# Optimization experiments

Measured on AMD Instinct MI355X. Metric: run time of the kernel, lower is better.

## Reference

```python
import jax, jax.numpy as jnp
import numpy as np

B, W, N = 4, 8, 1024
F_IN, HID, OUT = 256, 256, 128


def setup_inputs() -> dict:
    key = jax.random.key(0)
    ks = jax.random.split(key, 8)
    X = jax.random.normal(ks[0], (B, W, N, F_IN), dtype=jnp.float32)
    adj = jax.random.uniform(ks[1], (B, W, N, N), dtype=jnp.float32)
    # Linear params, torch default init: U(-1/sqrt(fan_in), 1/sqrt(fan_in))
    def lin(k, fi, fo):
        k1, k2 = jax.random.split(k)
        bnd = 1.0 / np.sqrt(fi)
        Wm = jax.random.uniform(k1, (fi, fo), minval=-bnd, maxval=bnd, dtype=jnp.float32)
        bm = jax.random.uniform(k2, (fo,), minval=-bnd, maxval=bnd, dtype=jnp.float32)
        return Wm, bm
    W1, b1 = lin(ks[2], F_IN, HID)
    W2, b2 = lin(ks[3], HID, HID)
    W3, b3 = lin(ks[4], HID, OUT)
    return {"X": X, "adj": adj, "W1": W1, "b1": b1, "W2": W2, "b2": b2, "W3": W3, "b3": b3}


def _normalize(adj):
    # adj: [B, W, N, N]. adj_hat = adj + I; sym degree norm D^-1/2 A D^-1/2
    n = adj.shape[-1]
    adj_hat = adj + jnp.eye(n, dtype=adj.dtype)
    d = jnp.sum(adj_hat, axis=-1) ** (-0.5)            # [B, W, N]
    # diag(d) @ adj_hat @ diag(d) == row/col scaling (same math, no N^3 diag matmuls)
    return adj_hat * d[..., :, None] * d[..., None, :]


def reference(X, adj, W1, b1, W2, b2, W3, b3):
    adj_norm = _normalize(adj)                          # [B, W, N, N]
    h = X
    for Wm, bm in ((W1, b1), (W2, b2), (W3, b3)):
        h = jnp.einsum('bwnm,bwmf->bwnf', adj_norm, h)  # aggregate
        h = jax.nn.relu(jnp.einsum('bwnf,fo->bwno', h, Wm) + bm)
    return h                                            # [B, W, N, OUT]
```

## Files before the change

### kernel.cpp

```cpp
#include <hip/hip_runtime.h>
#include <hip/hip_bf16.h>
#include <cstdint>
#include <cstddef>

#define NN 1024
#define FF 256

typedef __attribute__((ext_vector_type(8))) short bf16x8;
typedef __attribute__((ext_vector_type(4))) float f32x4;

__device__ __forceinline__ short f2bf(float x) {
  unsigned int u = __float_as_uint(x);
  u = (u + 0x7fffu + ((u >> 16) & 1u)) >> 16;
  return (short)u;
}


__global__ __launch_bounds__(256)
void dinv_cast(const float* __restrict__ adj, float* __restrict__ dinv,
               short* __restrict__ Ahat) {
  __shared__ float wsum[64];
  int b = blockIdx.x;
  int bw = b >> 6, s = b & 63;
  int t = threadIdx.x;
  int wid = t >> 6, lane = t & 63;
  int row = lane & 15;
  int rloc = (s << 4) + row;
  int kg = (lane >> 4) & 3;
  const float* arow = adj + ((size_t)(bw << 10) + rloc) * NN;
  short* outb = Ahat + ((size_t)bw << 20) + ((size_t)s << 14) + (t << 3);
  float ssum = 0.f;
  #pragma unroll
  for (int it = 0; it < 8; it++) {
    int col = (it << 7) + (wid << 5) + (kg << 3);
    float4 a0 = *(const float4*)(arow + col);
    float4 a1 = *(const float4*)(arow + col + 4);
    float v[8] = {a0.x, a0.y, a0.z, a0.w, a1.x, a1.y, a1.z, a1.w};
    union { ushort o[8]; int4 q; } pk;
    #pragma unroll
    for (int j = 0; j < 8; j++) {
      v[j] += (rloc == col + j) ? 1.f : 0.f;
      ssum += v[j];
      pk.o[j] = (ushort)f2bf(v[j]);
    }
    *(int4*)(outb + (it << 11)) = pk.q;
  }
  ssum += __shfl_down(ssum, 32, 64);
  ssum += __shfl_down(ssum, 16, 64);
  if (lane < 16) wsum[(wid << 4) + lane] = ssum;
  __syncthreads();
  if (t < 16) {
    float tot = wsum[t] + wsum[16 + t] + wsum[32 + t] + wsum[48 + t];
    dinv[(bw << 10) + (s << 4) + t] = rsqrtf(tot);
  }
}

__global__ __launch_bounds__(256)
void transpose_x(const float* __restrict__ X, const float* __restrict__ dinv,
                 short* __restrict__ XT) {
  __shared__ short T[64][72];
  int bwo = blockIdx.z;
  int n0 = blockIdx.x << 6, f0 = blockIdx.y << 6;
  int t = threadIdx.x;
  {
    int n = t >> 2, fc = (t & 3) << 4;
    float dn = dinv[(bwo << 10) + n0 + n];
    const float* src = X + (((size_t)bwo * NN + n0 + n) * FF) + f0 + fc;
    #pragma unroll
    for (int i = 0; i < 4; i++) {
      float4 v = ((const float4*)src)[i];
      ushort4 p;
      p.x = (unsigned short)f2bf(v.x * dn); p.y = (unsigned short)f2bf(v.y * dn);
      p.z = (unsigned short)f2bf(v.z * dn); p.w = (unsigned short)f2bf(v.w * dn);
      *(ushort4*)&T[n][fc + (i << 2)] = p;
    }
  }
  __syncthreads();
  {
    int f = t >> 2, nc = (t & 3) << 4;
    int fg = f0 + f, ng = n0 + nc;
    short tmp[16];
    #pragma unroll
    for (int i = 0; i < 16; i++) tmp[i] = T[nc + i][f];
    size_t e0 = ((size_t)bwo << 18) + ((size_t)(fg >> 4) << 14) + ((ng >> 5) << 9)
              + (((ng & 31) >> 3) << 7) + ((fg & 15) << 3);
    *(int4*)(XT + e0)       = *(int4*)&tmp[0];
    *(int4*)(XT + e0 + 128) = *(int4*)&tmp[8];
  }
}

__global__ __launch_bounds__(256)
void transpose_w(const float* __restrict__ W, short* __restrict__ WT, int FO) {
  int idx = blockIdx.x * 256 + threadIdx.x;
  if (idx >= FO * 256) return;
  int fo = idx >> 8, fi = idx & 255;
  size_t e = (size_t)((fo >> 4) << 12) + ((fi >> 5) << 9)
           + (((fi & 31) >> 3) << 7) + ((fo & 15) << 3) + (fi & 7);
  WT[e] = f2bf(W[fi * FO + fo]);
}

template<int F_OUT, bool FINAL>
__global__ __launch_bounds__(256, 3)
void gcn_layer(const short* __restrict__ Ahat,
               const float* __restrict__ dinv,
               const short* __restrict__ Gin,
               const short* __restrict__ WT,
               const float* __restrict__ bias,
               short* __restrict__ Gout,
               float* __restrict__ Out) {
  __shared__ short aggL[64 * 272];

  int b = blockIdx.x;
  int x = b & 7, m = b >> 3;
  int bw = (x << 2) + (m >> 4);
  int rb = m & 15;
  int r0 = rb << 6;

  int tid = threadIdx.x;
  int wf = tid >> 6, lane = tid & 63;
  int l15 = lane & 15, l4 = lane >> 4;

  const short* Hbase = Gin  + ((size_t)bw << 18) + ((size_t)(wf << 2) << 14) + (lane << 3);
  const short* Abase = Ahat + ((size_t)bw << 20) + ((size_t)(rb << 2) << 14) + (lane << 3);
  const float* dvB = dinv + (bw << 10);

  f32x4 acc[4][4];
  #pragma unroll
  for (int ah = 0; ah < 4; ah++)
    #pragma unroll
    for (int aa = 0; aa < 4; aa++) acc[ah][aa] = f32x4{0.f, 0.f, 0.f, 0.f};

  bf16x8 hE[4], aE[4], hO[4], aO[4];

#define LD(HB, AB, T)                                                         \
  {                                                                           \
    _Pragma("unroll")                                                         \
    for (int ah = 0; ah < 4; ah++)                                            \
      HB[ah] = *(const bf16x8*)(Hbase + ah * 16384 + (T) * 512);              \
    _Pragma("unroll")                                                         \
    for (int aa = 0; aa < 4; aa++)                                            \
      AB[aa] = *(const bf16x8*)(Abase + aa * 16384 + (T) * 512);              \
  }
#define MM(HB, AB)                                                            \
  __builtin_amdgcn_s_setprio(1);                                              \
  _Pragma("unroll")                                                           \
  for (int ah = 0; ah < 4; ah++)                                              \
    _Pragma("unroll")                                                         \
    for (int aa = 0; aa < 4; aa++)                                            \
      acc[ah][aa] = __builtin_amdgcn_mfma_f32_16x16x32_bf16(                  \
          HB[ah], AB[aa], acc[ah][aa], 0, 0, 0);                              \
  __builtin_amdgcn_s_setprio(0);

  LD(hE, aE, 0);
  LD(hO, aO, 1);
  #pragma unroll
  for (int it = 0; it < 16; ++it) {
    MM(hE, aE);
    if (it < 15) LD(hE, aE, 2 * it + 2);
    MM(hO, aO);
    if (it < 15) LD(hO, aO, 2 * it + 3);
  }
#undef LD
#undef MM

  float dsc[4];
  #pragma unroll
  for (int aa = 0; aa < 4; aa++) dsc[aa] = dvB[r0 + (aa << 4) + l15];
  #pragma unroll
  for (int ah = 0; ah < 4; ah++)
    #pragma unroll
    for (int aa = 0; aa < 4; aa++) {
      int r = (aa << 4) + l15;
      int fB = ((wf << 6) + (ah << 4) + (l4 << 2)) << 1;
      int off = (r * 544 + (fB ^ ((r & 7) << 4))) >> 1;
      ushort4 p;
      p.x = (unsigned short)f2bf(acc[ah][aa][0] * dsc[aa]);
      p.y = (unsigned short)f2bf(acc[ah][aa][1] * dsc[aa]);
      p.z = (unsigned short)f2bf(acc[ah][aa][2] * dsc[aa]);
      p.w = (unsigned short)f2bf(acc[ah][aa][3] * dsc[aa]);
      *(ushort4*)(aggL + off) = p;
    }
  __syncthreads();

  constexpr int NFO = F_OUT / 64;
  const short* Wbase = WT + (size_t)(wf * NFO) * 4096 + (lane << 3);
  f32x4 acc2[4][NFO];
  #pragma unroll
  for (int am = 0; am < 4; am++)
    #pragma unroll
    for (int nf = 0; nf < NFO; nf++) acc2[am][nf] = f32x4{0.f, 0.f, 0.f, 0.f};

  #pragma unroll
  for (int kt = 0; kt < 8; kt++) {
    bf16x8 af[4];
    #pragma unroll
    for (int am = 0; am < 4; am++) {
      int r = (am << 4) + l15;
      int fB = (kt << 6) + (l4 << 4);
      af[am] = *(const bf16x8*)(aggL + ((r * 544 + (fB ^ ((r & 7) << 4))) >> 1));
    }
    #pragma unroll
    for (int nf = 0; nf < NFO; nf++) {
      bf16x8 wv = *(const bf16x8*)(Wbase + (size_t)nf * 4096 + (kt << 9));
      #pragma unroll
      for (int am = 0; am < 4; am++)
        acc2[am][nf] = __builtin_amdgcn_mfma_f32_16x16x32_bf16(af[am], wv, acc2[am][nf], 0, 0, 0);
    }
  }

  #pragma unroll
  for (int am = 0; am < 4; am++) {
    int nodeLoc = (am << 4) + (l4 << 2);
    float4 dn4 = *(const float4*)(dvB + r0 + nodeLoc);
    float dn[4] = {dn4.x, dn4.y, dn4.z, dn4.w};
    #pragma unroll
    for (int nf = 0; nf < NFO; nf++) {
      int fo = wf * (F_OUT / 4) + (nf << 4) + l15;
      float bb = bias[fo];
      float v[4];
      #pragma unroll
      for (int j = 0; j < 4; j++) v[j] = fmaxf(acc2[am][nf][j] + bb, 0.f);
      if (!FINAL) {
        ushort4 p;
        p.x = (unsigned short)f2bf(v[0] * dn[0]);
        p.y = (unsigned short)f2bf(v[1] * dn[1]);
        p.z = (unsigned short)f2bf(v[2] * dn[2]);
        p.w = (unsigned short)f2bf(v[3] * dn[3]);
        size_t e = (size_t)bw * (F_OUT * 1024) + ((size_t)(fo >> 4) << 14)
                 + ((size_t)((rb << 1) + (am >> 1)) << 9)
                 + ((size_t)(((am & 1) << 1) + (l4 >> 1)) << 7)
                 + ((fo & 15) << 3) + ((l4 & 1) << 2);
        *(ushort4*)(Gout + e) = p;
      } else {
        float* ob = Out + ((size_t)(bw << 10) + r0 + nodeLoc) * F_OUT + fo;
        ob[0]         = v[0];
        ob[F_OUT]     = v[1];
        ob[2 * F_OUT] = v[2];
        ob[3 * F_OUT] = v[3];
      }
    }
  }
}

extern "C" void kernel_launch(void* const* d_in, const int* in_sizes, int n_in,
                              void* d_out, int out_size, void* d_ws, size_t ws_size,
                              hipStream_t stream) {
  const float* X   = (const float*)d_in[0];
  const float* adj = (const float*)d_in[1];
  const float* W1  = (const float*)d_in[2];
  const float* b1  = (const float*)d_in[3];
  const float* W2  = (const float*)d_in[4];
  const float* b2  = (const float*)d_in[5];
  const float* W3  = (const float*)d_in[6];
  const float* b3  = (const float*)d_in[7];
  float* out = (float*)d_out;

  char* ws = (char*)d_ws;
  float* dinv = (float*)ws;
  short* WT1  = (short*)(ws + 131072);
  short* WT2  = (short*)(ws + 262144);
  short* WT3  = (short*)(ws + 393216);
  short* bufA = (short*)(ws + 458752);
  short* bufB = (short*)(ws + 458752 + 16777216);
  short* Ahat = (short*)(ws + 458752 + 2 * 16777216);

  dinv_cast<<<2048, 256, 0, stream>>>(adj, dinv, Ahat);
  transpose_x<<<dim3(16, 4, 32), 256, 0, stream>>>(X, dinv, bufA);
  transpose_w<<<256, 256, 0, stream>>>(W1, WT1, 256);
  transpose_w<<<256, 256, 0, stream>>>(W2, WT2, 256);
  transpose_w<<<128, 256, 0, stream>>>(W3, WT3, 128);

  gcn_layer<256, false><<<512, 256, 0, stream>>>(Ahat, dinv, bufA, WT1, b1, bufB, nullptr);
  gcn_layer<256, false><<<512, 256, 0, stream>>>(Ahat, dinv, bufB, WT2, b2, bufA, nullptr);
  gcn_layer<128, true ><<<512, 256, 0, stream>>>(Ahat, dinv, bufA, WT3, b3, nullptr, out);
}
```

Measured before the change: 138.9 us.

## Double 128-row tiles per block and stage adjacency via global_load_lds

Each gcn_layer block now covers 128 rows using 512 threads (two row-groups of four waves), so every H tile loaded from global is reused across twice as many adjacency rows. Adjacency tiles are copied straight into double-buffered LDS with global_load_lds and shared across the row-group waves, with explicit waitcnt and barriers around each stage. The aim is to reduce redundant global traffic for H and A. The cost is half as many blocks (256), which leaves less parallelism on a large GPU, plus a barrier in every K step and heavier reliance on hand-placed waitcnt for correctness.

Result: slower. 148.5 us (+6.9%).

```diff
diff --git a/kernel.cpp b/kernel.cpp
--- a/kernel.cpp
+++ b/kernel.cpp
@@ -8,6 +8,9 @@
 
 typedef __attribute__((ext_vector_type(8))) short bf16x8;
 typedef __attribute__((ext_vector_type(4))) float f32x4;
+
+typedef __attribute__((address_space(1))) const void* gas_ptr;
+typedef __attribute__((address_space(3))) void* las_ptr;
 
 __device__ __forceinline__ short f2bf(float x) {
   unsigned int u = __float_as_uint(x);
@@ -100,7 +103,7 @@
 }
 
 template<int F_OUT, bool FINAL>
-__global__ __launch_bounds__(256, 3)
+__global__ __launch_bounds__(512, 2)
 void gcn_layer(const short* __restrict__ Ahat,
                const float* __restrict__ dinv,
                const short* __restrict__ Gin,
@@ -108,69 +111,86 @@
                const float* __restrict__ bias,
                short* __restrict__ Gout,
                float* __restrict__ Out) {
-  __shared__ short aggL[64 * 272];
+  __shared__ short lds[34816];
 
   int b = blockIdx.x;
   int x = b & 7, m = b >> 3;
-  int bw = (x << 2) + (m >> 4);
-  int rb = m & 15;
-  int r0 = rb << 6;
+  int bw = (x << 2) + (m >> 3);
+  int rb = m & 7;
+  int r0 = rb << 7;
 
   int tid = threadIdx.x;
-  int wf = tid >> 6, lane = tid & 63;
+  int wid = tid >> 6, lane = tid & 63;
   int l15 = lane & 15, l4 = lane >> 4;
-
-  const short* Hbase = Gin  + ((size_t)bw << 18) + ((size_t)(wf << 2) << 14) + (lane << 3);
-  const short* Abase = Ahat + ((size_t)bw << 20) + ((size_t)(rb << 2) << 14) + (lane << 3);
+  int wr = wid >> 2, wf = wid & 3;
+
+  const short* Hb = Gin + ((size_t)bw << 18) + ((size_t)(wf << 2) << 14) + (lane << 3);
   const float* dvB = dinv + (bw << 10);
 
+  auto stage = [&](int sel, int T) {
+    const short* gb = Ahat + ((size_t)bw << 20) + ((size_t)(T << 1) << 9);
+    short* dst = lds + (sel << 13);
+    #pragma unroll
+    for (int i = 0; i < 2; i++) {
+      int slot = (i << 9) + tid;
+      int s = slot >> 7, c = slot & 127;
+      const short* g = gb + ((size_t)((rb << 3) + s) << 14) + (c << 3);
+      __builtin_amdgcn_global_load_lds((gas_ptr)g, (las_ptr)(dst + (slot << 3)), 16, 0, 0);
+    }
+  };
+
   f32x4 acc[4][4];
   #pragma unroll
   for (int ah = 0; ah < 4; ah++)
     #pragma unroll
     for (int aa = 0; aa < 4; aa++) acc[ah][aa] = f32x4{0.f, 0.f, 0.f, 0.f};
 
-  bf16x8 hE[4], aE[4], hO[4], aO[4];
-
-#define LD(HB, AB, T)                                                         \
-  {                                                                           \
-    _Pragma("unroll")                                                         \
-    for (int ah = 0; ah < 4; ah++)                                            \
-      HB[ah] = *(const bf16x8*)(Hbase + ah * 16384 + (T) * 512);              \
-    _Pragma("unroll")                                                         \
-    for (int aa = 0; aa < 4; aa++)                                            \
-      AB[aa] = *(const bf16x8*)(Abase + aa * 16384 + (T) * 512);              \
-  }
-#define MM(HB, AB)                                                            \
-  __builtin_amdgcn_s_setprio(1);                                              \
-  _Pragma("unroll")                                                           \
-  for (int ah = 0; ah < 4; ah++)                                              \
-    _Pragma("unroll")                                                         \
-    for (int aa = 0; aa < 4; aa++)                                            \
-      acc[ah][aa] = __builtin_amdgcn_mfma_f32_16x16x32_bf16(                  \
-          HB[ah], AB[aa], acc[ah][aa], 0, 0, 0);                              \
-  __builtin_amdgcn_s_setprio(0);
-
-  LD(hE, aE, 0);
-  LD(hO, aO, 1);
-  #pragma unroll
-  for (int it = 0; it < 16; ++it) {
-    MM(hE, aE);
-    if (it < 15) LD(hE, aE, 2 * it + 2);
-    MM(hO, aO);
-    if (it < 15) LD(hO, aO, 2 * it + 3);
-  }
-#undef LD
-#undef MM
+  stage(0, 0);
+
+  for (int t = 0; t < 16; ++t) {
+    bf16x8 h[4][2];
+    #pragma unroll
+    for (int fh = 0; fh < 4; fh++) {
+      h[fh][0] = *(const bf16x8*)(Hb + ((size_t)fh << 14) + ((size_t)(2 * t) << 9));
+      h[fh][1] = *(const bf16x8*)(Hb + ((size_t)fh << 14) + ((size_t)(2 * t + 1) << 9));
+    }
+    asm volatile("s_waitcnt vmcnt(8)" ::: "memory");
+    __builtin_amdgcn_sched_barrier(0);
+    __builtin_amdgcn_s_barrier();
+    __builtin_amdgcn_sched_barrier(0);
+    if (t < 15) stage((t + 1) & 1, t + 1);
+    const short* ab = lds + ((t & 1) << 13);
+    bf16x8 a[4][2];
+    #pragma unroll
+    for (int aa = 0; aa < 4; aa++) {
+      int sa = (wr << 2) + aa;
+      a[aa][0] = *(const bf16x8*)(ab + (sa << 10) + (lane << 3));
+      a[aa][1] = *(const bf16x8*)(ab + (sa << 10) + 512 + (lane << 3));
+    }
+    __builtin_amdgcn_s_setprio(1);
+    #pragma unroll
+    for (int kt = 0; kt < 2; kt++)
+      #pragma unroll
+      for (int ah = 0; ah < 4; ah++)
+        #pragma unroll
+        for (int aa = 0; aa < 4; aa++)
+          acc[ah][aa] = __builtin_amdgcn_mfma_f32_16x16x32_bf16(
+              h[ah][kt], a[aa][kt], acc[ah][aa], 0, 0, 0);
+    __builtin_amdgcn_s_setprio(0);
+  }
+
+  __builtin_amdgcn_sched_barrier(0);
+  __builtin_amdgcn_s_barrier();
+  __builtin_amdgcn_sched_barrier(0);
 
   float dsc[4];
   #pragma unroll
-  for (int aa = 0; aa < 4; aa++) dsc[aa] = dvB[r0 + (aa << 4) + l15];
+  for (int aa = 0; aa < 4; aa++) dsc[aa] = dvB[r0 + (wr << 6) + (aa << 4) + l15];
   #pragma unroll
   for (int ah = 0; ah < 4; ah++)
     #pragma unroll
     for (int aa = 0; aa < 4; aa++) {
-      int r = (aa << 4) + l15;
+      int r = (wr << 6) + (aa << 4) + l15;
       int fB = ((wf << 6) + (ah << 4) + (l4 << 2)) << 1;
       int off = (r * 544 + (fB ^ ((r & 7) << 4))) >> 1;
       ushort4 p;
@@ -178,9 +198,12 @@
       p.y = (unsigned short)f2bf(acc[ah][aa][1] * dsc[aa]);
       p.z = (unsigned short)f2bf(acc[ah][aa][2] * dsc[aa]);
       p.w = (unsigned short)f2bf(acc[ah][aa][3] * dsc[aa]);
-      *(ushort4*)(aggL + off) = p;
-    }
-  __syncthreads();
+      *(ushort4*)(lds + off) = p;
+    }
+  asm volatile("s_waitcnt lgkmcnt(0)" ::: "memory");
+  __builtin_amdgcn_sched_barrier(0);
+  __builtin_amdgcn_s_barrier();
+  __builtin_amdgcn_sched_barrier(0);
 
   constexpr int NFO = F_OUT / 64;
   const short* Wbase = WT + (size_t)(wf * NFO) * 4096 + (lane << 3);
@@ -195,9 +218,9 @@
     bf16x8 af[4];
     #pragma unroll
     for (int am = 0; am < 4; am++) {
-      int r = (am << 4) + l15;
+      int r = (wr << 6) + (am << 4) + l15;
       int fB = (kt << 6) + (l4 << 4);
-      af[am] = *(const bf16x8*)(aggL + ((r * 544 + (fB ^ ((r & 7) << 4))) >> 1));
+      af[am] = *(const bf16x8*)(lds + ((r * 544 + (fB ^ ((r & 7) << 4))) >> 1));
     }
     #pragma unroll
     for (int nf = 0; nf < NFO; nf++) {
@@ -210,7 +233,7 @@
 
   #pragma unroll
   for (int am = 0; am < 4; am++) {
-    int nodeLoc = (am << 4) + (l4 << 2);
+    int nodeLoc = (wr << 6) + (am << 4) + (l4 << 2);
     float4 dn4 = *(const float4*)(dvB + r0 + nodeLoc);
     float dn[4] = {dn4.x, dn4.y, dn4.z, dn4.w};
     #pragma unroll
@@ -227,7 +250,7 @@
         p.z = (unsigned short)f2bf(v[2] * dn[2]);
         p.w = (unsigned short)f2bf(v[3] * dn[3]);
         size_t e = (size_t)bw * (F_OUT * 1024) + ((size_t)(fo >> 4) << 14)
-                 + ((size_t)((rb << 1) + (am >> 1)) << 9)
+                 + ((size_t)((rb << 2) + (wr << 1) + (am >> 1)) << 9)
                  + ((size_t)(((am & 1) << 1) + (l4 >> 1)) << 7)
                  + ((fo & 15) << 3) + ((l4 & 1) << 2);
         *(ushort4*)(Gout + e) = p;
@@ -270,7 +293,7 @@
   transpose_w<<<256, 256, 0, stream>>>(W2, WT2, 256);
   transpose_w<<<128, 256, 0, stream>>>(W3, WT3, 128);
 
-  gcn_layer<256, false><<<512, 256, 0, stream>>>(Ahat, dinv, bufA, WT1, b1, bufB, nullptr);
-  gcn_layer<256, false><<<512, 256, 0, stream>>>(Ahat, dinv, bufB, WT2, b2, bufA, nullptr);
-  gcn_layer<128, true ><<<512, 256, 0, stream>>>(Ahat, dinv, bufA, WT3, b3, nullptr, out);
-}
+  gcn_layer<256, false><<<256, 512, 0, stream>>>(Ahat, dinv, bufA, WT1, b1, bufB, nullptr);
+  gcn_layer<256, false><<<256, 512, 0, stream>>>(Ahat, dinv, bufB, WT2, b2, bufA, nullptr);
+  gcn_layer<128, true ><<<256, 512, 0, stream>>>(Ahat, dinv, bufA, WT3, b3, nullptr, out);
+}
```
